# Optimization experiments

Measured on AMD Instinct MI355X. Metric: run time of the kernel, lower is better.

The kernel has to match this reference:

```python
import jax, jax.numpy as jnp
from jax import lax
import numpy as np

F_IN, F_OUT, T = 32, 64, 8
H1 = (3 * F_IN + F_OUT) // 4  # 40
H2 = F_OUT                    # 64
N, E = 50000, 800000


def setup_inputs() -> dict:
    key = jax.random.key(0)
    ks = jax.random.split(key, 8)
    def p(k, shape, fan_in):
        return jax.random.normal(k, shape, jnp.float32) / np.float32(np.sqrt(fan_in))
    return {
        "temporal_features": jax.random.normal(ks[0], (N, F_IN, T), jnp.float32),
        "src": jax.random.randint(ks[1], (E,), 0, N, jnp.int32),
        "dst": jax.random.randint(ks[2], (E,), 0, N, jnp.int32),
        "W1": p(ks[3], (F_IN, H1), F_IN), "b1": jnp.zeros((H1,), jnp.float32),
        "W2": p(ks[4], (H1, H2), H1),   "b2": jnp.zeros((H2,), jnp.float32),
        "W3": p(ks[5], (H2, F_OUT), H2), "b3": jnp.zeros((F_OUT,), jnp.float32),
        "Wc": p(ks[6], (F_OUT, F_OUT, 3), F_OUT * 3),  # Conv1d weight [out, in, k]
        "bc": jnp.zeros((F_OUT,), jnp.float32),
    }


def _graph_conv(h, src, dst, out_norm, in_norm, W, b, act, n):
    # dgl GraphConv, norm='both': D_out^{-1/2} -> sum-aggregate -> D_in^{-1/2} -> linear
    h = h * out_norm[:, None, None]                       # [N, t, f]
    agg = jax.ops.segment_sum(h[src], dst, num_segments=n)  # irregular gather/scatter
    h = agg * in_norm[:, None, None]
    h = jnp.einsum("nti,io->nto", h, W) + b
    return jax.nn.relu(h) if act else h


def reference(temporal_features, src, dst, W1, b1, W2, b2, W3, b3, Wc, bc):
    n = temporal_features.shape[0]
    ones = jnp.ones(src.shape, temporal_features.dtype)
    out_deg = jax.ops.segment_sum(ones, src, num_segments=n)
    in_deg = jax.ops.segment_sum(ones, dst, num_segments=n)
    out_norm = jnp.clip(out_deg, 1.0, None) ** -0.5
    in_norm = jnp.clip(in_deg, 1.0, None) ** -0.5

    h = jnp.swapaxes(temporal_features, -2, -1)  # [N, t, f_in]
    h = _graph_conv(h, src, dst, out_norm, in_norm, W1, b1, True, n)
    h = _graph_conv(h, src, dst, out_norm, in_norm, W2, b2, True, n)
    h = _graph_conv(h, src, dst, out_norm, in_norm, W3, b3, False, n)
    h = jnp.swapaxes(h, -2, -1)  # [N, f_out, t]

    out = lax.conv_general_dilated(
        h, Wc, window_strides=(1,), padding=((1, 1),),
        dimension_numbers=("NCH", "OIH", "NCH"))
    return out + bc[None, :, None]
```

## Files before the change

kernel.cpp:

```cpp
#include <hip/hip_runtime.h>


__global__ __launch_bounds__(256) void deg_kernel(const int* __restrict__ src,
                                                  const int* __restrict__ dst,
                                                  int* __restrict__ out_deg,
                                                  int* __restrict__ in_deg, int E) {
  int e = blockIdx.x * 256 + threadIdx.x;
  if (e < E) {
    atomicAdd(&out_deg[src[e]], 1);
    atomicAdd(&in_deg[dst[e]], 1);
  }
}

__global__ __launch_bounds__(256) void norm_kernel(const int* __restrict__ out_deg,
                                                   const int* __restrict__ in_deg,
                                                   float* __restrict__ out_norm,
                                                   float* __restrict__ in_norm, int N) {
  int n = blockIdx.x * 256 + threadIdx.x;
  if (n < N) {
    out_norm[n] = 1.0f / sqrtf((float)max(out_deg[n], 1));
    in_norm[n]  = 1.0f / sqrtf((float)max(in_deg[n], 1));
  }
}

__global__ __launch_bounds__(256) void wct_kernel(const float* __restrict__ Wc,
                                                  float* __restrict__ wct) {
  int m = blockIdx.x * 256 + threadIdx.x;
  if (m < 12288) wct[m] = Wc[(m & 63) * 192 + (m >> 6)];
}


__global__ __launch_bounds__(256) void scan_partial_kernel(const int* __restrict__ deg,
                                                           int* __restrict__ partial, int N) {
  __shared__ int ws[4];
  int tid = threadIdx.x, lane = tid & 63, wv = tid >> 6;
  int base = blockIdx.x * 1024;
  int v = 0;
#pragma unroll
  for (int k = 0; k < 4; ++k) {
    int i = base + tid + k * 256;
    if (i < N) v += deg[i];
  }
  for (int d = 32; d > 0; d >>= 1) v += __shfl_down(v, d, 64);
  if (lane == 0) ws[wv] = v;
  __syncthreads();
  if (tid == 0) partial[blockIdx.x] = ws[0] + ws[1] + ws[2] + ws[3];
}

__global__ __launch_bounds__(1024) void scan_partials_kernel(int* __restrict__ partial, int P) {
  __shared__ int wsum[16];
  int tid = threadIdx.x, lane = tid & 63, wv = tid >> 6;
  int v = (tid < P) ? partial[tid] : 0;
  int x = v;
  for (int d = 1; d < 64; d <<= 1) {
    int y = __shfl_up(x, d, 64);
    if (lane >= d) x += y;
  }
  if (lane == 63) wsum[wv] = x;
  __syncthreads();
  if (wv == 0 && lane < 16) {
    int y = wsum[lane];
    int z = y;
    for (int d = 1; d < 16; d <<= 1) {
      int q = __shfl_up(z, d, 64);
      if (lane >= d) z += q;
    }
    wsum[lane] = z - y;
  }
  __syncthreads();
  if (tid < P) partial[tid] = wsum[wv] + x - v;
}

__global__ __launch_bounds__(1024) void scan_apply_kernel(const int* __restrict__ deg,
                                                          const int* __restrict__ partial,
                                                          int* __restrict__ off, int N) {
  __shared__ int wsum[16];
  int tid = threadIdx.x, lane = tid & 63, wv = tid >> 6;
  int i = blockIdx.x * 1024 + tid;
  int v = (i < N) ? deg[i] : 0;
  int x = v;
  for (int d = 1; d < 64; d <<= 1) {
    int y = __shfl_up(x, d, 64);
    if (lane >= d) x += y;
  }
  if (lane == 63) wsum[wv] = x;
  __syncthreads();
  if (wv == 0 && lane < 16) {
    int y = wsum[lane];
    int z = y;
    for (int d = 1; d < 16; d <<= 1) {
      int q = __shfl_up(z, d, 64);
      if (lane >= d) z += q;
    }
    wsum[lane] = z - y;
  }
  __syncthreads();
  int excl = partial[blockIdx.x] + wsum[wv] + (x - v);
  if (i < N) off[i] = excl;
  if (i == N - 1) off[N] = excl + v;
}

__global__ __launch_bounds__(256) void scatter_kernel(const int* __restrict__ src,
                                                      const int* __restrict__ dst,
                                                      const int* __restrict__ in_off,
                                                      int* __restrict__ cursor,
                                                      int* __restrict__ csr_src, int E) {
  int e = blockIdx.x * 256 + threadIdx.x;
  if (e < E) {
    int d = dst[e];
    int p = atomicAdd(&cursor[d], 1);
    csr_src[in_off[d] + p] = src[e];
  }
}

template <int F_IN, int F_OUT, int TS, int L, bool IT_LAYOUT, bool RELU,
          bool GNORM, bool SCALE_OUT, int WPE>
__device__ __forceinline__ void layer_body(
    const float* __restrict__ h_in, const int* __restrict__ csr_src,
    const int* __restrict__ in_off, const float* __restrict__ out_norm,
    const float* __restrict__ in_norm, const float* __restrict__ W,
    const float* __restrict__ bias, float* __restrict__ h_out, int N) {
  constexpr int NF4 = F_IN * 2;
  constexpr int NC = NF4 / L;
  constexpr int M = 64 / L;
  constexpr int SLOTS = 4 * M;
  constexpr int SLOT = IT_LAYOUT ? F_IN * 8 : TS * 8;
  __shared__ float agg[SLOTS][SLOT];
  int tid = threadIdx.x;
  int wave = tid >> 6, lane = tid & 63;
  int q = lane / L, r = lane % L;
  int slot = wave * M + q;
  int n = blockIdx.x * SLOTS + slot;
  bool valid = (n < N);

  float4 acc[NC];
#pragma unroll
  for (int k = 0; k < NC; ++k) acc[k] = make_float4(0.f, 0.f, 0.f, 0.f);

  if (valid) {
    int e0 = in_off[n], e1 = in_off[n + 1];
    const float4* h4 = (const float4*)h_in;
    int j = e0;
    if (e1 - e0 >= 2) {
      int sA = csr_src[j], sB = csr_src[j + 1];
      do {
        int cA = sA, cB = sB;
        int jn = j + 2;
        sA = csr_src[min(jn, e1 - 1)];
        sB = csr_src[min(jn + 1, e1 - 1)];
        float wA = 1.f, wB = 1.f;
        if constexpr (GNORM) { wA = out_norm[cA]; wB = out_norm[cB]; }
        const float4* pA = h4 + (size_t)cA * NF4 + r;
        const float4* pB = h4 + (size_t)cB * NF4 + r;
        float4 vA[NC], vB[NC];
#pragma unroll
        for (int k = 0; k < NC; ++k) vA[k] = pA[k * L];
#pragma unroll
        for (int k = 0; k < NC; ++k) vB[k] = pB[k * L];
#pragma unroll
        for (int k = 0; k < NC; ++k) {
          acc[k].x = fmaf(vA[k].x, wA, acc[k].x);
          acc[k].y = fmaf(vA[k].y, wA, acc[k].y);
          acc[k].z = fmaf(vA[k].z, wA, acc[k].z);
          acc[k].w = fmaf(vA[k].w, wA, acc[k].w);
          acc[k].x = fmaf(vB[k].x, wB, acc[k].x);
          acc[k].y = fmaf(vB[k].y, wB, acc[k].y);
          acc[k].z = fmaf(vB[k].z, wB, acc[k].z);
          acc[k].w = fmaf(vB[k].w, wB, acc[k].w);
        }
        j = jn;
      } while (j + 2 <= e1);
    }
    if (j < e1) {
      int s = csr_src[j];
      float w = 1.f;
      if constexpr (GNORM) w = out_norm[s];
      const float4* p = h4 + (size_t)s * NF4 + r;
#pragma unroll
      for (int k = 0; k < NC; ++k) {
        float4 v = p[k * L];
        acc[k].x = fmaf(v.x, w, acc[k].x);
        acc[k].y = fmaf(v.y, w, acc[k].y);
        acc[k].z = fmaf(v.z, w, acc[k].z);
        acc[k].w = fmaf(v.w, w, acc[k].w);
      }
    }
    float innm = in_norm[n];
#pragma unroll
    for (int k = 0; k < NC; ++k) {
      int el = (k * L + r) * 4;
      int addr;
      if constexpr (IT_LAYOUT || TS == F_IN) {
        addr = el;
      } else {
        int t = el / F_IN;
        int i = el - t * F_IN;
        addr = t * TS + i;
      }
      *(float4*)&agg[slot][addr] = make_float4(acc[k].x * innm, acc[k].y * innm,
                                               acc[k].z * innm, acc[k].w * innm);
    }
  }

  constexpr int G = F_OUT / 8;
  int t = lane >> 3, og = lane & 7;
  float acc2[M][G];
  {
    float bb[G];
    if constexpr (G == 8) {
      float4 bA = *(const float4*)&bias[og * 8];
      float4 bB = *(const float4*)&bias[og * 8 + 4];
      bb[0] = bA.x; bb[1] = bA.y; bb[2] = bA.z; bb[3] = bA.w;
      bb[4] = bB.x; bb[5] = bB.y; bb[6] = bB.z; bb[7] = bB.w;
    } else {
#pragma unroll
      for (int c = 0; c < G; ++c) bb[c] = bias[og * G + c];
    }
#pragma unroll
    for (int qq = 0; qq < M; ++qq)
#pragma unroll
      for (int c = 0; c < G; ++c) acc2[qq][c] = bb[c];
  }
#pragma unroll 4
  for (int i = 0; i < F_IN; ++i) {
    float wrow[G];
    if constexpr (G == 8) {
      float4 wA = *(const float4*)&W[i * F_OUT + og * 8];
      float4 wB = *(const float4*)&W[i * F_OUT + og * 8 + 4];
      wrow[0] = wA.x; wrow[1] = wA.y; wrow[2] = wA.z; wrow[3] = wA.w;
      wrow[4] = wB.x; wrow[5] = wB.y; wrow[6] = wB.z; wrow[7] = wB.w;
    } else {
#pragma unroll
      for (int c = 0; c < G; ++c) wrow[c] = W[i * F_OUT + og * G + c];
    }
    int raddr;
    if constexpr (IT_LAYOUT) raddr = i * 8 + t;
    else raddr = t * TS + i;
#pragma unroll
    for (int qq = 0; qq < M; ++qq) {
      float a = agg[wave * M + qq][raddr];
#pragma unroll
      for (int c = 0; c < G; ++c) acc2[qq][c] = fmaf(a, wrow[c], acc2[qq][c]);
    }
  }
#pragma unroll
  for (int qq = 0; qq < M; ++qq) {
    int n2 = blockIdx.x * SLOTS + wave * M + qq;
    if (n2 < N) {
      float osc = 1.f;
      if constexpr (SCALE_OUT) osc = out_norm[n2];
      float res[G];
#pragma unroll
      for (int c = 0; c < G; ++c) {
        float v = acc2[qq][c];
        if constexpr (RELU) v = fmaxf(v, 0.f);
        res[c] = v * osc;
      }
      float* orow = h_out + (size_t)n2 * (F_OUT * 8) + t * F_OUT + og * G;
      if constexpr (G == 8) {
        *(float4*)&orow[0] = make_float4(res[0], res[1], res[2], res[3]);
        *(float4*)&orow[4] = make_float4(res[4], res[5], res[6], res[7]);
      } else {
#pragma unroll
        for (int c = 0; c < G; ++c) orow[c] = res[c];
      }
    }
  }
}

__global__ __launch_bounds__(256, 5) void layer1_k(
    const float* __restrict__ h_in, const int* __restrict__ csr_src,
    const int* __restrict__ in_off, const float* __restrict__ out_norm,
    const float* __restrict__ in_norm, const float* __restrict__ W,
    const float* __restrict__ bias, float* __restrict__ h_out, int N) {
  layer_body<32, 40, 0, 8, true, true, true, true, 5>(
      h_in, csr_src, in_off, out_norm, in_norm, W, bias, h_out, N);
}

__global__ __launch_bounds__(256, 6) void layer2_k(
    const float* __restrict__ h_in, const int* __restrict__ csr_src,
    const int* __restrict__ in_off, const float* __restrict__ out_norm,
    const float* __restrict__ in_norm, const float* __restrict__ W,
    const float* __restrict__ bias, float* __restrict__ h_out, int N) {
  layer_body<40, 64, 40, 16, false, true, false, true, 6>(
      h_in, csr_src, in_off, out_norm, in_norm, W, bias, h_out, N);
}

__global__ __launch_bounds__(256, 4) void layer3_conv_k(
    const float* __restrict__ h_in, const int* __restrict__ csr_src,
    const int* __restrict__ in_off, const float* __restrict__ in_norm,
    const float* __restrict__ W, const float* __restrict__ bias,
    const float* __restrict__ wct, const float* __restrict__ bc,
    float* __restrict__ out, int N) {
  __shared__ float agg[16][512];
  int tid = threadIdx.x;
  int wave = tid >> 6, lane = tid & 63;
  int q = lane >> 4, r = lane & 15;
  int slot = wave * 4 + q;
  int n = blockIdx.x * 16 + slot;
  bool valid = (n < N);

  float4 acc[8];
#pragma unroll
  for (int k = 0; k < 8; ++k) acc[k] = make_float4(0.f, 0.f, 0.f, 0.f);

  if (valid) {
    int e0 = in_off[n], e1 = in_off[n + 1];
    const float4* h4 = (const float4*)h_in;
    int j = e0;
    if (e1 - e0 >= 2) {
      int sA = csr_src[j], sB = csr_src[j + 1];
      do {
        int cA = sA, cB = sB;
        int jn = j + 2;
        sA = csr_src[min(jn, e1 - 1)];
        sB = csr_src[min(jn + 1, e1 - 1)];
        const float4* pA = h4 + (size_t)cA * 128 + r;
        const float4* pB = h4 + (size_t)cB * 128 + r;
        float4 vA[8], vB[8];
#pragma unroll
        for (int k = 0; k < 8; ++k) vA[k] = pA[k * 16];
#pragma unroll
        for (int k = 0; k < 8; ++k) vB[k] = pB[k * 16];
#pragma unroll
        for (int k = 0; k < 8; ++k) {
          acc[k].x += vA[k].x + vB[k].x;
          acc[k].y += vA[k].y + vB[k].y;
          acc[k].z += vA[k].z + vB[k].z;
          acc[k].w += vA[k].w + vB[k].w;
        }
        j = jn;
      } while (j + 2 <= e1);
    }
    if (j < e1) {
      int s = csr_src[j];
      const float4* p = h4 + (size_t)s * 128 + r;
#pragma unroll
      for (int k = 0; k < 8; ++k) {
        float4 v = p[k * 16];
        acc[k].x += v.x; acc[k].y += v.y; acc[k].z += v.z; acc[k].w += v.w;
      }
    }
    float innm = in_norm[n];
#pragma unroll
    for (int k = 0; k < 8; ++k) {
      int f4i = k * 16 + (r ^ k);
      *(float4*)&agg[slot][f4i * 4] = make_float4(acc[k].x * innm, acc[k].y * innm,
                                                  acc[k].z * innm, acc[k].w * innm);
    }
  }

  int t = lane >> 3, og = lane & 7;
  float acc2[4][8];
  {
    float4 bA = *(const float4*)&bias[og * 8];
    float4 bB = *(const float4*)&bias[og * 8 + 4];
    float bb[8] = {bA.x, bA.y, bA.z, bA.w, bB.x, bB.y, bB.z, bB.w};
#pragma unroll
    for (int qq = 0; qq < 4; ++qq)
#pragma unroll
      for (int c = 0; c < 8; ++c) acc2[qq][c] = bb[c];
  }
  int tb = t * 64;
#pragma unroll 4
  for (int i = 0; i < 64; ++i) {
    float4 wA = *(const float4*)&W[i * 64 + og * 8];
    float4 wB = *(const float4*)&W[i * 64 + og * 8 + 4];
    float wrow[8] = {wA.x, wA.y, wA.z, wA.w, wB.x, wB.y, wB.z, wB.w};
    int raddr = tb + (((i >> 2) ^ t) << 2) + (i & 3);
#pragma unroll
    for (int qq = 0; qq < 4; ++qq) {
      float a = agg[wave * 4 + qq][raddr];
#pragma unroll
      for (int c = 0; c < 8; ++c) acc2[qq][c] = fmaf(a, wrow[c], acc2[qq][c]);
    }
  }

#pragma unroll
  for (int qq = 0; qq < 4; ++qq) {
    float* sb = &agg[wave * 4 + qq][og * 64 + t];
#pragma unroll
    for (int c = 0; c < 8; ++c) sb[(c ^ (og & 3)) << 3] = acc2[qq][c];
  }

  float4 b4 = *(const float4*)&bc[r * 4];
  float bcv[4] = {b4.x, b4.y, b4.z, b4.w};
  float cacc[4][8];
#pragma unroll
  for (int c = 0; c < 4; ++c)
#pragma unroll
    for (int tt = 0; tt < 8; ++tt) cacc[c][tt] = bcv[c];

  const float4* wct4 = (const float4*)wct;
  const float* hq = &agg[wave * 4 + q][0];
#pragma unroll 2
  for (int i = 0; i < 64; ++i) {
    int ib = i >> 3, ic = i & 7;
    const float* hi = &hq[ib * 64 + ((ic ^ (ib & 3)) << 3)];
    float4 hA = *(const float4*)hi;
    float4 hB = *(const float4*)(hi + 4);
    float4 w0 = wct4[(i * 3 + 0) * 16 + r];
    float4 w1 = wct4[(i * 3 + 1) * 16 + r];
    float4 w2 = wct4[(i * 3 + 2) * 16 + r];
    float h[8] = {hA.x, hA.y, hA.z, hA.w, hB.x, hB.y, hB.z, hB.w};
    float wk0[4] = {w0.x, w0.y, w0.z, w0.w};
    float wk1[4] = {w1.x, w1.y, w1.z, w1.w};
    float wk2[4] = {w2.x, w2.y, w2.z, w2.w};
#pragma unroll
    for (int c = 0; c < 4; ++c) {
#pragma unroll
      for (int tt = 0; tt < 8; ++tt) cacc[c][tt] = fmaf(wk1[c], h[tt], cacc[c][tt]);
#pragma unroll
      for (int tt = 1; tt < 8; ++tt) cacc[c][tt] = fmaf(wk0[c], h[tt - 1], cacc[c][tt]);
#pragma unroll
      for (int tt = 0; tt < 7; ++tt) cacc[c][tt] = fmaf(wk2[c], h[tt + 1], cacc[c][tt]);
    }
  }
  if (valid) {
    float* ob = out + (size_t)n * 512 + r * 32;
#pragma unroll
    for (int c = 0; c < 4; ++c) {
      *(float4*)&ob[c * 8] = make_float4(cacc[c][0], cacc[c][1], cacc[c][2], cacc[c][3]);
      *(float4*)&ob[c * 8 + 4] = make_float4(cacc[c][4], cacc[c][5], cacc[c][6], cacc[c][7]);
    }
  }
}


extern "C" void kernel_launch(void* const* d_in, const int* in_sizes, int n_in,
                              void* d_out, int out_size, void* d_ws, size_t ws_size,
                              hipStream_t stream) {
  const float* tf = (const float*)d_in[0];
  const int* src = (const int*)d_in[1];
  const int* dst = (const int*)d_in[2];
  const float* W1 = (const float*)d_in[3];
  const float* b1 = (const float*)d_in[4];
  const float* W2 = (const float*)d_in[5];
  const float* b2 = (const float*)d_in[6];
  const float* W3 = (const float*)d_in[7];
  const float* b3 = (const float*)d_in[8];
  const float* Wc = (const float*)d_in[9];
  const float* bc = (const float*)d_in[10];

  int N = in_sizes[0] / 256;
  int E = in_sizes[1];

  char* ws = (char*)d_ws;
  size_t pos = 0;
  auto alloc = [&](size_t bytes) -> void* {
    void* p = ws + pos;
    pos += (bytes + 255) & ~(size_t)255;
    return p;
  };
  int* in_deg   = (int*)alloc((size_t)N * 4);
  int* out_deg  = (int*)alloc((size_t)N * 4);
  int* cursor   = (int*)alloc((size_t)N * 4);
  int* in_off   = (int*)alloc((size_t)(N + 1) * 4);
  int* partial  = (int*)alloc((size_t)1024 * 4);
  float* o_norm = (float*)alloc((size_t)N * 4);
  float* i_norm = (float*)alloc((size_t)N * 4);
  int* csr      = (int*)alloc((size_t)E * 4);
  float* wct    = (float*)alloc((size_t)12288 * 4);
  float* h1     = (float*)alloc((size_t)N * 320 * 4);
  float* h2     = (float*)alloc((size_t)N * 512 * 4);

  hipMemsetAsync(in_deg, 0, (size_t)((char*)in_off - (char*)in_deg), stream);

  deg_kernel<<<(E + 255) / 256, 256, 0, stream>>>(src, dst, out_deg, in_deg, E);
  norm_kernel<<<(N + 255) / 256, 256, 0, stream>>>(out_deg, in_deg, o_norm, i_norm, N);
  wct_kernel<<<48, 256, 0, stream>>>(Wc, wct);

  int P = (N + 1023) / 1024;
  scan_partial_kernel<<<P, 256, 0, stream>>>(in_deg, partial, N);
  scan_partials_kernel<<<1, 1024, 0, stream>>>(partial, P);
  scan_apply_kernel<<<P, 1024, 0, stream>>>(in_deg, partial, in_off, N);

  scatter_kernel<<<(E + 255) / 256, 256, 0, stream>>>(src, dst, in_off, cursor, csr, E);

  layer1_k<<<(N + 31) / 32, 256, 0, stream>>>(tf, csr, in_off, o_norm, i_norm, W1, b1, h1, N);
  layer2_k<<<(N + 15) / 16, 256, 0, stream>>>(h1, csr, in_off, o_norm, i_norm, W2, b2, h2, N);
  layer3_conv_k<<<(N + 15) / 16, 256, 0, stream>>>(h2, csr, in_off, i_norm, W3, b3,
                                                   wct, bc, (float*)d_out, N);
}
```

Baseline: 888.0 us.

## Shrink per-block node count and pad shared slots to raise occupancy

Layer 3 now processes 8 nodes per block with 32 lanes per node instead of 16 nodes with 16 lanes, which halves the per-thread accumulators and shared memory and raises the occupancy hint. Shared-memory rows gain padding (stride 68, +8 per slot) in place of XOR swizzles to avoid bank conflicts. Layer 1 changes lane grouping from 8 to 16 per node, and layer 2 gets a padded time stride. The intent is more waves in flight to hide gather latency, at the cost of more blocks and the extra per-block overhead of weight loads.

Result: no change. 882.0 us (-0.7%).

```diff
diff --git a/kernel.cpp b/kernel.cpp
--- a/kernel.cpp
+++ b/kernel.cpp
@@ -114,7 +114,7 @@
 }
 
 template <int F_IN, int F_OUT, int TS, int L, bool IT_LAYOUT, bool RELU,
-          bool GNORM, bool SCALE_OUT, int WPE>
+          bool GNORM, bool SCALE_OUT>
 __device__ __forceinline__ void layer_body(
     const float* __restrict__ h_in, const int* __restrict__ csr_src,
     const int* __restrict__ in_off, const float* __restrict__ out_norm,
@@ -124,7 +124,7 @@
   constexpr int NC = NF4 / L;
   constexpr int M = 64 / L;
   constexpr int SLOTS = 4 * M;
-  constexpr int SLOT = IT_LAYOUT ? F_IN * 8 : TS * 8;
+  constexpr int SLOT = (IT_LAYOUT ? F_IN * 8 : TS * 8) + 8;
   __shared__ float agg[SLOTS][SLOT];
   int tid = threadIdx.x;
   int wave = tid >> 6, lane = tid & 63;
@@ -190,7 +190,7 @@
     for (int k = 0; k < NC; ++k) {
       int el = (k * L + r) * 4;
       int addr;
-      if constexpr (IT_LAYOUT || TS == F_IN) {
+      if constexpr (IT_LAYOUT) {
         addr = el;
       } else {
         int t = el / F_IN;
@@ -268,12 +268,12 @@
   }
 }
 
-__global__ __launch_bounds__(256, 5) void layer1_k(
+__global__ __launch_bounds__(256, 7) void layer1_k(
     const float* __restrict__ h_in, const int* __restrict__ csr_src,
     const int* __restrict__ in_off, const float* __restrict__ out_norm,
     const float* __restrict__ in_norm, const float* __restrict__ W,
     const float* __restrict__ bias, float* __restrict__ h_out, int N) {
-  layer_body<32, 40, 0, 8, true, true, true, true, 5>(
+  layer_body<32, 40, 0, 16, true, true, true, true>(
       h_in, csr_src, in_off, out_norm, in_norm, W, bias, h_out, N);
 }
 
@@ -282,27 +282,28 @@
     const int* __restrict__ in_off, const float* __restrict__ out_norm,
     const float* __restrict__ in_norm, const float* __restrict__ W,
     const float* __restrict__ bias, float* __restrict__ h_out, int N) {
-  layer_body<40, 64, 40, 16, false, true, false, true, 6>(
+  layer_body<40, 64, 44, 16, false, true, false, true>(
       h_in, csr_src, in_off, out_norm, in_norm, W, bias, h_out, N);
 }
 
-__global__ __launch_bounds__(256, 4) void layer3_conv_k(
+__global__ __launch_bounds__(256, 7) void layer3_conv_k(
     const float* __restrict__ h_in, const int* __restrict__ csr_src,
     const int* __restrict__ in_off, const float* __restrict__ in_norm,
     const float* __restrict__ W, const float* __restrict__ bias,
     const float* __restrict__ wct, const float* __restrict__ bc,
     float* __restrict__ out, int N) {
-  __shared__ float agg[16][512];
+  constexpr int SLOT = 8 * 68 + 8;
+  __shared__ float agg[8][SLOT];
   int tid = threadIdx.x;
   int wave = tid >> 6, lane = tid & 63;
-  int q = lane >> 4, r = lane & 15;
-  int slot = wave * 4 + q;
-  int n = blockIdx.x * 16 + slot;
+  int q = lane >> 5, r = lane & 31;
+  int slot = wave * 2 + q;
+  int n = blockIdx.x * 8 + slot;
   bool valid = (n < N);
 
-  float4 acc[8];
-#pragma unroll
-  for (int k = 0; k < 8; ++k) acc[k] = make_float4(0.f, 0.f, 0.f, 0.f);
+  float4 acc[4];
+#pragma unroll
+  for (int k = 0; k < 4; ++k) acc[k] = make_float4(0.f, 0.f, 0.f, 0.f);
 
   if (valid) {
     int e0 = in_off[n], e1 = in_off[n + 1];
@@ -317,13 +318,13 @@
         sB = csr_src[min(jn + 1, e1 - 1)];
         const float4* pA = h4 + (size_t)cA * 128 + r;
         const float4* pB = h4 + (size_t)cB * 128 + r;
-        float4 vA[8], vB[8];
-#pragma unroll
-        for (int k = 0; k < 8; ++k) vA[k] = pA[k * 16];
-#pragma unroll
-        for (int k = 0; k < 8; ++k) vB[k] = pB[k * 16];
-#pragma unroll
-        for (int k = 0; k < 8; ++k) {
+        float4 vA[4], vB[4];
+#pragma unroll
+        for (int k = 0; k < 4; ++k) vA[k] = pA[k * 32];
+#pragma unroll
+        for (int k = 0; k < 4; ++k) vB[k] = pB[k * 32];
+#pragma unroll
+        for (int k = 0; k < 4; ++k) {
           acc[k].x += vA[k].x + vB[k].x;
           acc[k].y += vA[k].y + vB[k].y;
           acc[k].z += vA[k].z + vB[k].z;
@@ -336,78 +337,76 @@
       int s = csr_src[j];
       const float4* p = h4 + (size_t)s * 128 + r;
 #pragma unroll
-      for (int k = 0; k < 8; ++k) {
-        float4 v = p[k * 16];
+      for (int k = 0; k < 4; ++k) {
+        float4 v = p[k * 32];
         acc[k].x += v.x; acc[k].y += v.y; acc[k].z += v.z; acc[k].w += v.w;
       }
     }
     float innm = in_norm[n];
 #pragma unroll
-    for (int k = 0; k < 8; ++k) {
-      int f4i = k * 16 + (r ^ k);
-      *(float4*)&agg[slot][f4i * 4] = make_float4(acc[k].x * innm, acc[k].y * innm,
-                                                  acc[k].z * innm, acc[k].w * innm);
+    for (int k = 0; k < 4; ++k) {
+      int t0 = 2 * k + (r >> 4);
+      int addr = t0 * 68 + ((r & 15) << 2);
+      *(float4*)&agg[slot][addr] = make_float4(acc[k].x * innm, acc[k].y * innm,
+                                               acc[k].z * innm, acc[k].w * innm);
     }
   }
 
   int t = lane >> 3, og = lane & 7;
-  float acc2[4][8];
+  float acc2[2][8];
   {
     float4 bA = *(const float4*)&bias[og * 8];
     float4 bB = *(const float4*)&bias[og * 8 + 4];
     float bb[8] = {bA.x, bA.y, bA.z, bA.w, bB.x, bB.y, bB.z, bB.w};
 #pragma unroll
-    for (int qq = 0; qq < 4; ++qq)
+    for (int qq = 0; qq < 2; ++qq)
 #pragma unroll
       for (int c = 0; c < 8; ++c) acc2[qq][c] = bb[c];
   }
-  int tb = t * 64;
 #pragma unroll 4
   for (int i = 0; i < 64; ++i) {
     float4 wA = *(const float4*)&W[i * 64 + og * 8];
     float4 wB = *(const float4*)&W[i * 64 + og * 8 + 4];
     float wrow[8] = {wA.x, wA.y, wA.z, wA.w, wB.x, wB.y, wB.z, wB.w};
-    int raddr = tb + (((i >> 2) ^ t) << 2) + (i & 3);
-#pragma unroll
-    for (int qq = 0; qq < 4; ++qq) {
-      float a = agg[wave * 4 + qq][raddr];
+    int raddr = t * 68 + i;
+#pragma unroll
+    for (int qq = 0; qq < 2; ++qq) {
+      float a = agg[wave * 2 + qq][raddr];
 #pragma unroll
       for (int c = 0; c < 8; ++c) acc2[qq][c] = fmaf(a, wrow[c], acc2[qq][c]);
     }
   }
 
 #pragma unroll
-  for (int qq = 0; qq < 4; ++qq) {
-    float* sb = &agg[wave * 4 + qq][og * 64 + t];
-#pragma unroll
-    for (int c = 0; c < 8; ++c) sb[(c ^ (og & 3)) << 3] = acc2[qq][c];
-  }
-
-  float4 b4 = *(const float4*)&bc[r * 4];
-  float bcv[4] = {b4.x, b4.y, b4.z, b4.w};
-  float cacc[4][8];
-#pragma unroll
-  for (int c = 0; c < 4; ++c)
-#pragma unroll
-    for (int tt = 0; tt < 8; ++tt) cacc[c][tt] = bcv[c];
-
-  const float4* wct4 = (const float4*)wct;
-  const float* hq = &agg[wave * 4 + q][0];
+  for (int qq = 0; qq < 2; ++qq) {
+    float* sb = &agg[wave * 2 + qq][og * 64 + t];
+#pragma unroll
+    for (int c = 0; c < 8; ++c) sb[((c + og) & 7) << 3] = acc2[qq][c];
+  }
+
+  int q2 = lane >> 5, s = lane & 31;
+  float2 b2v = *(const float2*)&bc[s * 2];
+  float cacc[2][8];
+#pragma unroll
+  for (int tt = 0; tt < 8; ++tt) { cacc[0][tt] = b2v.x; cacc[1][tt] = b2v.y; }
+
+  const float2* wct2 = (const float2*)wct;
+  const float* hq = &agg[wave * 2 + q2][0];
 #pragma unroll 2
   for (int i = 0; i < 64; ++i) {
     int ib = i >> 3, ic = i & 7;
-    const float* hi = &hq[ib * 64 + ((ic ^ (ib & 3)) << 3)];
+    const float* hi = &hq[ib * 64 + (((ic + ib) & 7) << 3)];
     float4 hA = *(const float4*)hi;
     float4 hB = *(const float4*)(hi + 4);
-    float4 w0 = wct4[(i * 3 + 0) * 16 + r];
-    float4 w1 = wct4[(i * 3 + 1) * 16 + r];
-    float4 w2 = wct4[(i * 3 + 2) * 16 + r];
+    float2 w0 = wct2[(i * 3 + 0) * 32 + s];
+    float2 w1 = wct2[(i * 3 + 1) * 32 + s];
+    float2 w2 = wct2[(i * 3 + 2) * 32 + s];
     float h[8] = {hA.x, hA.y, hA.z, hA.w, hB.x, hB.y, hB.z, hB.w};
-    float wk0[4] = {w0.x, w0.y, w0.z, w0.w};
-    float wk1[4] = {w1.x, w1.y, w1.z, w1.w};
-    float wk2[4] = {w2.x, w2.y, w2.z, w2.w};
-#pragma unroll
-    for (int c = 0; c < 4; ++c) {
+    float wk0[2] = {w0.x, w0.y};
+    float wk1[2] = {w1.x, w1.y};
+    float wk2[2] = {w2.x, w2.y};
+#pragma unroll
+    for (int c = 0; c < 2; ++c) {
 #pragma unroll
       for (int tt = 0; tt < 8; ++tt) cacc[c][tt] = fmaf(wk1[c], h[tt], cacc[c][tt]);
 #pragma unroll
@@ -416,10 +415,11 @@
       for (int tt = 0; tt < 7; ++tt) cacc[c][tt] = fmaf(wk2[c], h[tt + 1], cacc[c][tt]);
     }
   }
-  if (valid) {
-    float* ob = out + (size_t)n * 512 + r * 32;
-#pragma unroll
-    for (int c = 0; c < 4; ++c) {
+  int n2 = blockIdx.x * 8 + wave * 2 + q2;
+  if (n2 < N) {
+    float* ob = out + (size_t)n2 * 512 + s * 16;
+#pragma unroll
+    for (int c = 0; c < 2; ++c) {
       *(float4*)&ob[c * 8] = make_float4(cacc[c][0], cacc[c][1], cacc[c][2], cacc[c][3]);
       *(float4*)&ob[c * 8 + 4] = make_float4(cacc[c][4], cacc[c][5], cacc[c][6], cacc[c][7]);
     }
@@ -477,8 +477,8 @@
 
   scatter_kernel<<<(E + 255) / 256, 256, 0, stream>>>(src, dst, in_off, cursor, csr, E);
 
-  layer1_k<<<(N + 31) / 32, 256, 0, stream>>>(tf, csr, in_off, o_norm, i_norm, W1, b1, h1, N);
+  layer1_k<<<(N + 15) / 16, 256, 0, stream>>>(tf, csr, in_off, o_norm, i_norm, W1, b1, h1, N);
   layer2_k<<<(N + 15) / 16, 256, 0, stream>>>(h1, csr, in_off, o_norm, i_norm, W2, b2, h2, N);
-  layer3_conv_k<<<(N + 15) / 16, 256, 0, stream>>>(h2, csr, in_off, i_norm, W3, b3,
-                                                   wct, bc, (float*)d_out, N);
-}
+  layer3_conv_k<<<(N + 7) / 8, 256, 0, stream>>>(h2, csr, in_off, i_norm, W3, b3,
+                                                 wct, bc, (float*)d_out, N);
+}
```
